# Optimization experiments

Hardware: AMD Instinct MI355X
Metric: run time of the kernel (lower is better)

Reference implementation:

```python
import jax, jax.numpy as jnp
import numpy as np

NHEAD = 8

def setup_inputs() -> dict:
    key = jax.random.key(0)
    ks = jax.random.split(key, 7)
    B, N, D = 8, 1024, 512
    scale = 1.0 / np.sqrt(D)
    return {
        "x": jax.random.normal(ks[0], (B, N, D), dtype=jnp.float32),
        "graph_bias": jax.random.normal(ks[1], (B, N, N), dtype=jnp.float32),
        "in_proj_w": jax.random.normal(ks[2], (3 * D, D), dtype=jnp.float32) * scale,
        "in_proj_b": jax.random.normal(ks[3], (3 * D,), dtype=jnp.float32) * 0.02,
        "out_proj_w": jax.random.normal(ks[4], (D, D), dtype=jnp.float32) * scale,
        "out_proj_b": jax.random.normal(ks[5], (D,), dtype=jnp.float32) * 0.02,
        "bias_strength": jnp.ones((), dtype=jnp.float32),
    }

def reference(x, graph_bias, in_proj_w, in_proj_b, out_proj_w, out_proj_b, bias_strength):
    B, N, D = x.shape
    H = NHEAD
    hd = D // H
    # fused QKV projection (matches nn.MultiheadAttention in_proj)
    qkv = x @ in_proj_w.T + in_proj_b          # (B, N, 3D)
    q, k, v = jnp.split(qkv, 3, axis=-1)
    # (B, H, N, hd)
    q = q.reshape(B, N, H, hd).transpose(0, 2, 1, 3)
    k = k.reshape(B, N, H, hd).transpose(0, 2, 1, 3)
    v = v.reshape(B, N, H, hd).transpose(0, 2, 1, 3)
    # additive bias from predicted causal structure
    alpha = jax.nn.sigmoid(bias_strength)
    causal_mask = jax.nn.sigmoid(graph_bias).transpose(0, 2, 1)   # (B, N, N)
    causal_mask = alpha * causal_mask + (1.0 - alpha) * 0.5
    attn_bias = (causal_mask - 0.5) * 10.0                        # (B, N, N)
    scores = jnp.einsum("bhqd,bhkd->bhqk", q, k) / jnp.sqrt(jnp.asarray(hd, x.dtype))
    scores = scores + attn_bias[:, None, :, :]                    # broadcast over heads
    probs = jax.nn.softmax(scores, axis=-1)
    out = jnp.einsum("bhqk,bhkd->bhqd", probs, v)                 # (B, H, N, hd)
    out = out.transpose(0, 2, 1, 3).reshape(B, N, D)
    return out @ out_proj_w.T + out_proj_b
```

## Files before the change

### kernel.cpp

```cpp
#include <hip/hip_runtime.h>

typedef __attribute__((ext_vector_type(8))) __bf16 bf16x8;
typedef __attribute__((ext_vector_type(4))) __bf16 bf16x4;
typedef __attribute__((ext_vector_type(4))) float f32x4;
typedef __attribute__((ext_vector_type(8))) _Float16 f16x8;

#define LOG2E 1.44269504088896340736f

__device__ __forceinline__ void async_load16(const void* g, void* l) {
  __builtin_amdgcn_global_load_lds(
      (const __attribute__((address_space(1))) void*)g,
      (__attribute__((address_space(3))) void*)l, 16, 0, 0);
}

__device__ __forceinline__ float fast_exp2(float x) {
#if __has_builtin(__builtin_amdgcn_exp2f)
  return __builtin_amdgcn_exp2f(x);
#else
  return __expf(x * 0.6931471805599453f);
#endif
}

__global__ void cvt3(const float* __restrict__ a, __bf16* __restrict__ oa, int na4,
                     const float* __restrict__ b, __bf16* __restrict__ ob, int nb4,
                     const float* __restrict__ c, __bf16* __restrict__ oc, int nc4) {
  int i = blockIdx.x * blockDim.x + threadIdx.x;
  int n = na4 + nb4 + nc4;
  int stride = gridDim.x * blockDim.x;
  for (; i < n; i += stride) {
    const float4* s;
    bf16x4* d;
    int j;
    if (i < na4) { s = (const float4*)a; d = (bf16x4*)oa; j = i; }
    else if (i < na4 + nb4) { s = (const float4*)b; d = (bf16x4*)ob; j = i - na4; }
    else { s = (const float4*)c; d = (bf16x4*)oc; j = i - na4 - nb4; }
    float4 v = s[j];
    bf16x4 o;
    o[0] = (__bf16)v.x; o[1] = (__bf16)v.y; o[2] = (__bf16)v.z; o[3] = (__bf16)v.w;
    d[j] = o;
  }
}

__global__ __launch_bounds__(256) void build_ebias(
    const float* __restrict__ gbias, const float* __restrict__ bstr,
    _Float16* __restrict__ ebT) {
  const int gid = blockIdx.x * 256 + threadIdx.x;
  const int lane = gid & 63;
  const int kt = (gid >> 6) & 31;
  const int qt = (gid >> 11) & 63;
  const int b = gid >> 17;
  const int g = lane >> 4, ln = lane & 15;
  const float alpha = 1.f / (1.f + __expf(-bstr[0]));
  const float bsc = 10.f * alpha * LOG2E;
  const float* base = gbias + (size_t)(b * 1024 + kt * 32 + ln) * 1024 + qt * 16 + g * 4;
  float4 va = *(const float4*)(base);
  float4 vb = *(const float4*)(base + 16 * 1024);
  float sv[8] = {va.x, va.y, va.z, va.w, vb.x, vb.y, vb.z, vb.w};
  f16x8 o;
#pragma unroll
  for (int i = 0; i < 8; ++i)
    o[i] = (_Float16)((1.f / (1.f + __expf(-sv[i])) - 0.5f) * bsc);
  *(f16x8*)(ebT + (size_t)gid * 8) = o;
}

template <int MODE>
__global__ __launch_bounds__(256) void gemm_bt(
    const __bf16* __restrict__ A, const __bf16* __restrict__ Bm,
    const float* __restrict__ bias, void* __restrict__ C0,
    __bf16* __restrict__ vT, int M, int N, int K) {
  __shared__ __align__(16) char smem[32768];
  char* lA = smem;
  char* lB = smem + 16384;
  const int t = threadIdx.x;
  const int lane = t & 63;
  const int wid = t >> 6;
  const int wm = wid >> 1, wn = wid & 1;
  const int g = lane >> 4, ln = lane & 15;
  const int m0 = blockIdx.y * 128;
  const int n0 = blockIdx.x * 128;

  const int srow = t >> 3;
  const int sswz = ((t & 7) * 16) ^ ((srow & 7) << 4);
  const size_t KB = (size_t)K * 2;
  const char* gA = (const char*)A + (size_t)m0 * KB;
  const char* gB = (const char*)Bm + (size_t)n0 * KB;

  f32x4 acc[4][4] = {};

  for (int k0 = 0; k0 < K; k0 += 64) {
    __syncthreads();
#pragma unroll
    for (int c = 0; c < 4; ++c) {
      int row = srow + 32 * c;
      async_load16(gA + (size_t)row * KB + k0 * 2 + sswz, lA + c * 4096 + t * 16);
      async_load16(gB + (size_t)row * KB + k0 * 2 + sswz, lB + c * 4096 + t * 16);
    }
    __syncthreads();
#pragma unroll
    for (int ks = 0; ks < 2; ++ks) {
      bf16x8 af[4], bf[4];
#pragma unroll
      for (int i = 0; i < 4; ++i) {
        int ar = wm * 64 + i * 16 + ln;
        int byo = (ks * 64 + g * 16) ^ ((ar & 7) << 4);
        af[i] = *(const bf16x8*)(lA + ar * 128 + byo);
        int br = wn * 64 + i * 16 + ln;
        bf[i] = *(const bf16x8*)(lB + br * 128 + byo);
      }
#pragma unroll
      for (int i = 0; i < 4; ++i)
#pragma unroll
        for (int j = 0; j < 4; ++j)
          acc[i][j] = __builtin_amdgcn_mfma_f32_16x16x32_bf16(af[i], bf[j], acc[i][j], 0, 0, 0);
    }
  }

#pragma unroll
  for (int j = 0; j < 4; ++j) {
    int col = n0 + wn * 64 + j * 16 + ln;
    float bv = bias[col];
    if (MODE == 0) {
#pragma unroll
      for (int i = 0; i < 4; ++i) {
        int row0 = m0 + wm * 64 + i * 16 + g * 4;
#pragma unroll
        for (int r = 0; r < 4; ++r)
          ((float*)C0)[(size_t)(row0 + r) * N + col] = acc[i][j][r] + bv;
      }
    } else if (col < 1024) {
      float scale = (col < 512) ? (0.125f * LOG2E) : 1.0f;
#pragma unroll
      for (int i = 0; i < 4; ++i) {
        int row0 = m0 + wm * 64 + i * 16 + g * 4;
#pragma unroll
        for (int r = 0; r < 4; ++r)
          ((__bf16*)C0)[(size_t)(row0 + r) * 1024 + col] = (__bf16)((acc[i][j][r] + bv) * scale);
      }
    } else {
      int h = (col - 1024) >> 6;
      int d = (col - 1024) & 63;
#pragma unroll
      for (int i = 0; i < 4; ++i) {
        int row0 = m0 + wm * 64 + i * 16 + g * 4;
        int b = row0 >> 10;
        bf16x4 pk;
#pragma unroll
        for (int r = 0; r < 4; ++r) pk[r] = (__bf16)(acc[i][j][r] + bv);
        *(bf16x4*)(vT + (((size_t)b * 8 + h) * 64 + d) * 1024 + (row0 & 1023)) = pk;
      }
    }
  }
}

__global__ __launch_bounds__(512, 4) void attn_fused(
    const __bf16* __restrict__ qk,
    const __bf16* __restrict__ vT,
    const _Float16* __restrict__ ebT,
    __bf16* __restrict__ attn) {
  __shared__ __align__(16) char smem[24576];
  const int t = threadIdx.x;
  const int lane = t & 63;
  const int wid = t >> 6;
  const int g = lane >> 4, ln = lane & 15;
  const int wg = ((blockIdx.x & 7) << 6) + (blockIdx.x >> 3);
  const int b = wg >> 6;
  const int rem = wg & 63;
  const int h = rem >> 3;
  const int qg = rem & 7;
  const int qt = qg * 8 + wid;
  const int q0 = qt << 4;

  char* K0 = smem;
  char* K1 = smem + 4096;
  char* V0 = smem + 8192;
  char* V1 = smem + 12288;
  char* Ps = smem + 16384 + wid * 1024;

  bf16x8 qf[2];
#pragma unroll
  for (int ks = 0; ks < 2; ++ks)
    qf[ks] = *(const bf16x8*)(qk + ((size_t)b * 1024 + q0 + ln) * 1024 +
                              h * 64 + ks * 32 + g * 8);

  float l_acc[4] = {0.f, 0.f, 0.f, 0.f};
  f32x4 o_acc[4] = {};

  const int krow = lane >> 3;
  const int ksrc = ((lane & 7) * 16) ^ (krow << 4);
  const int vrow = lane >> 2;
  const int vsrc = ((lane & 3) * 16) ^ ((vrow & 3) << 4);

  const char* qkb = (const char*)qk + (size_t)b * 1024 * 2048;
  const char* vTb = (const char*)vT + (size_t)(b * 8 + h) * 64 * 2048;
  const _Float16* ebp = ebT + (size_t)((b * 64 + qt) * 32) * 512 + lane * 8;

  auto stage = [&](int kt, char* Kd, char* Vd) {
    if (wid < 4) {
      async_load16(qkb + (size_t)(kt * 32 + wid * 8 + krow) * 2048 + 1024 + h * 128 + ksrc,
                   Kd + wid * 1024 + lane * 16);
    } else {
      int c = wid - 4;
      async_load16(vTb + (size_t)(c * 16 + vrow) * 2048 + (size_t)(kt * 32) * 2 + vsrc,
                   Vd + c * 1024 + lane * 16);
    }
  };

  stage(0, K0, V0);
  f16x8 ebc = *(const f16x8*)(ebp);
  f16x8 ebn = *(const f16x8*)(ebp + 512);
  asm volatile("s_waitcnt vmcnt(0)" ::: "memory");
  __syncthreads();

  for (int kt = 0; kt < 32; ++kt) {
    char* Kp = (kt & 1) ? K1 : K0;
    char* Vp = (kt & 1) ? V1 : V0;
    char* Kn = (kt & 1) ? K0 : K1;
    char* Vn = (kt & 1) ? V0 : V1;
    const int ktn = (kt + 1) & 31;
    const int kt2 = (kt + 2) & 31;

    stage(ktn, Kn, Vn);
    __builtin_amdgcn_sched_barrier(0);
    f16x8 ebn2 = *(const f16x8*)(ebp + (size_t)kt2 * 512);
    __builtin_amdgcn_sched_barrier(0);

    bf16x8 kf[2][2];
#pragma unroll
    for (int ni = 0; ni < 2; ++ni) {
      int br = ni * 16 + ln;
      int sw = (br & 7) << 4;
#pragma unroll
      for (int ks = 0; ks < 2; ++ks)
        kf[ni][ks] = *(const bf16x8*)(Kp + br * 128 + ((ks * 64 + g * 16) ^ sw));
    }
    bf16x8 vf[4];
#pragma unroll
    for (int di = 0; di < 4; ++di)
      vf[di] = *(const bf16x8*)(Vp + (di * 16 + ln) * 64 + ((g * 16) ^ ((ln & 3) << 4)));

    f32x4 lbf0 = {(float)ebc[0], (float)ebc[1], (float)ebc[2], (float)ebc[3]};
    f32x4 lbf1 = {(float)ebc[4], (float)ebc[5], (float)ebc[6], (float)ebc[7]};
    f32x4 s[2];
    s[0] = __builtin_amdgcn_mfma_f32_16x16x32_bf16(qf[0], kf[0][0], lbf0, 0, 0, 0);
    s[0] = __builtin_amdgcn_mfma_f32_16x16x32_bf16(qf[1], kf[0][1], s[0], 0, 0, 0);
    s[1] = __builtin_amdgcn_mfma_f32_16x16x32_bf16(qf[0], kf[1][0], lbf1, 0, 0, 0);
    s[1] = __builtin_amdgcn_mfma_f32_16x16x32_bf16(qf[1], kf[1][1], s[1], 0, 0, 0);

#pragma unroll
    for (int r = 0; r < 4; ++r) {
      float p0 = fast_exp2(s[0][r]);
      float p1 = fast_exp2(s[1][r]);
      s[0][r] = p0; s[1][r] = p1;
      l_acc[r] += p0 + p1;
    }
#pragma unroll
    for (int ni = 0; ni < 2; ++ni)
#pragma unroll
      for (int r = 0; r < 4; ++r) {
        int q = g * 4 + r;
        *(__bf16*)(Ps + q * 64 + ((ni * 32 + ln * 2) ^ (((q >> 1) & 3) << 4))) =
            (__bf16)s[ni][r];
      }
    bf16x8 pf = *(const bf16x8*)(Ps + ln * 64 + ((g * 16) ^ (((ln >> 1) & 3) << 4)));

#pragma unroll
    for (int di = 0; di < 4; ++di)
      o_acc[di] = __builtin_amdgcn_mfma_f32_16x16x32_bf16(pf, vf[di], o_acc[di], 0, 0, 0);

    asm volatile("s_waitcnt vmcnt(1)" ::: "memory");
    __builtin_amdgcn_sched_barrier(0);
    __syncthreads();
    ebc = ebn;
    ebn = ebn2;
  }

#pragma unroll
  for (int r = 0; r < 4; ++r) {
    float rs = l_acc[r];
#pragma unroll
    for (int off = 1; off < 16; off <<= 1)
      rs += __shfl_xor(rs, off, 64);
    float inv = 1.f / rs;
    int q = q0 + g * 4 + r;
#pragma unroll
    for (int di = 0; di < 4; ++di)
      attn[((size_t)b * 1024 + q) * 512 + h * 64 + di * 16 + ln] =
          (__bf16)(o_acc[di][r] * inv);
  }
}

extern "C" void kernel_launch(void* const* d_in, const int* in_sizes, int n_in,
                              void* d_out, int out_size, void* d_ws, size_t ws_size,
                              hipStream_t stream) {
  const float* x     = (const float*)d_in[0];
  const float* gb    = (const float*)d_in[1];
  const float* w_in  = (const float*)d_in[2];
  const float* b_in  = (const float*)d_in[3];
  const float* w_out = (const float*)d_in[4];
  const float* b_out = (const float*)d_in[5];
  const float* bstr  = (const float*)d_in[6];

  char* ws = (char*)d_ws;
  __bf16* qk    = (__bf16*)(ws);
  __bf16* vT    = (__bf16*)(ws + 16777216);
  __bf16* xb    = (__bf16*)(ws + 25165824);
  __bf16* w1    = (__bf16*)(ws + 33554432);
  __bf16* w2    = (__bf16*)(ws + 35127296);
  _Float16* ebT = (_Float16*)(ws + 35651584);
  __bf16* attn_buf = xb;

  cvt3<<<2560, 256, 0, stream>>>(x, xb, (8 * 1024 * 512) / 4,
                                 w_in, w1, (1536 * 512) / 4,
                                 w_out, w2, (512 * 512) / 4);
  build_ebias<<<4096, 256, 0, stream>>>(gb, bstr, ebT);

  gemm_bt<1><<<dim3(12, 64), 256, 0, stream>>>(xb, w1, b_in, qk, vT, 8192, 1536, 512);
  attn_fused<<<512, 512, 0, stream>>>(qk, vT, ebT, attn_buf);
  gemm_bt<0><<<dim3(4, 64), 256, 0, stream>>>(attn_buf, w2, b_out, d_out, nullptr, 8192, 512, 512);
}
```

Measured before the change: 96.16 us.

## Split attention key range across two wave groups and merge partial results in LDS

Each workgroup now handles 4 query tiles instead of 8, and its 8 waves split into two groups that each process half of the key tiles with their own double-buffered K/V staging. The second group writes its partial output and row sums to shared memory, and the first group adds them in before normalising and storing. The grid doubles to 1024 blocks to raise parallelism and shorten each wave's serial loop. In exchange, LDS per block grows, occupancy may drop, and K/V tiles are loaded with half the reuse across query tiles.

```diff
diff --git a/kernel.cpp b/kernel.cpp
--- a/kernel.cpp
+++ b/kernel.cpp
@@ -157,24 +157,28 @@
     const __bf16* __restrict__ vT,
     const _Float16* __restrict__ ebT,
     __bf16* __restrict__ attn) {
-  __shared__ __align__(16) char smem[24576];
+  __shared__ __align__(16) char smem[40960];
   const int t = threadIdx.x;
   const int lane = t & 63;
   const int wid = t >> 6;
   const int g = lane >> 4, ln = lane & 15;
-  const int wg = ((blockIdx.x & 7) << 6) + (blockIdx.x >> 3);
-  const int b = wg >> 6;
-  const int rem = wg & 63;
-  const int h = rem >> 3;
-  const int qg = rem & 7;
-  const int qt = qg * 8 + wid;
+  const int wg = ((blockIdx.x & 7) << 7) + (blockIdx.x >> 3);
+  const int b = wg >> 7;
+  const int rem = wg & 127;
+  const int h = rem >> 4;
+  const int qg = rem & 15;
+  const int qx = wid & 3;
+  const int kp = wid >> 2;
+  const int qt = qg * 4 + qx;
   const int q0 = qt << 4;
-
-  char* K0 = smem;
-  char* K1 = smem + 4096;
-  char* V0 = smem + 8192;
-  char* V1 = smem + 12288;
-  char* Ps = smem + 16384 + wid * 1024;
+  const int kt0 = kp * 16;
+
+  char* half = smem + kp * 16384;
+  char* K0 = half;
+  char* K1 = half + 4096;
+  char* V0 = half + 8192;
+  char* V1 = half + 12288;
+  char* Ps = smem + 32768 + wid * 1024;
 
   bf16x8 qf[2];
 #pragma unroll
@@ -194,30 +198,26 @@
   const char* vTb = (const char*)vT + (size_t)(b * 8 + h) * 64 * 2048;
   const _Float16* ebp = ebT + (size_t)((b * 64 + qt) * 32) * 512 + lane * 8;
 
-  auto stage = [&](int kt, char* Kd, char* Vd) {
-    if (wid < 4) {
-      async_load16(qkb + (size_t)(kt * 32 + wid * 8 + krow) * 2048 + 1024 + h * 128 + ksrc,
-                   Kd + wid * 1024 + lane * 16);
-    } else {
-      int c = wid - 4;
-      async_load16(vTb + (size_t)(c * 16 + vrow) * 2048 + (size_t)(kt * 32) * 2 + vsrc,
-                   Vd + c * 1024 + lane * 16);
-    }
+  auto stage = [&](int ktg, char* Kd, char* Vd) {
+    async_load16(qkb + (size_t)(ktg * 32 + qx * 8 + krow) * 2048 + 1024 + h * 128 + ksrc,
+                 Kd + qx * 1024 + lane * 16);
+    async_load16(vTb + (size_t)(qx * 16 + vrow) * 2048 + (size_t)(ktg * 32) * 2 + vsrc,
+                 Vd + qx * 1024 + lane * 16);
   };
 
-  stage(0, K0, V0);
-  f16x8 ebc = *(const f16x8*)(ebp);
-  f16x8 ebn = *(const f16x8*)(ebp + 512);
+  stage(kt0, K0, V0);
+  f16x8 ebc = *(const f16x8*)(ebp + (size_t)kt0 * 512);
+  f16x8 ebn = *(const f16x8*)(ebp + (size_t)(kt0 + 1) * 512);
   asm volatile("s_waitcnt vmcnt(0)" ::: "memory");
   __syncthreads();
 
-  for (int kt = 0; kt < 32; ++kt) {
+  for (int kt = 0; kt < 16; ++kt) {
     char* Kp = (kt & 1) ? K1 : K0;
     char* Vp = (kt & 1) ? V1 : V0;
     char* Kn = (kt & 1) ? K0 : K1;
     char* Vn = (kt & 1) ? V0 : V1;
-    const int ktn = (kt + 1) & 31;
-    const int kt2 = (kt + 2) & 31;
+    const int ktn = kt0 + ((kt + 1) & 15);
+    const int kt2 = kt0 + ((kt + 2) & 15);
 
     stage(ktn, Kn, Vn);
     __builtin_amdgcn_sched_barrier(0);
@@ -274,18 +274,40 @@
     ebn = ebn2;
   }
 
-#pragma unroll
-  for (int r = 0; r < 4; ++r) {
-    float rs = l_acc[r];
-#pragma unroll
-    for (int off = 1; off < 16; off <<= 1)
-      rs += __shfl_xor(rs, off, 64);
-    float inv = 1.f / rs;
-    int q = q0 + g * 4 + r;
+  if (kp == 1) {
+    char* dst = smem + 16384 + qx * 4096;
 #pragma unroll
     for (int di = 0; di < 4; ++di)
-      attn[((size_t)b * 1024 + q) * 512 + h * 64 + di * 16 + ln] =
-          (__bf16)(o_acc[di][r] * inv);
+      *(f32x4*)(dst + di * 1024 + lane * 16) = o_acc[di];
+    f32x4 lv = {l_acc[0], l_acc[1], l_acc[2], l_acc[3]};
+    *(f32x4*)(Ps + lane * 16) = lv;
+  }
+  __syncthreads();
+  if (kp == 0) {
+    const char* src = smem + 16384 + qx * 4096;
+#pragma unroll
+    for (int di = 0; di < 4; ++di) {
+      f32x4 ov = *(const f32x4*)(src + di * 1024 + lane * 16);
+#pragma unroll
+      for (int r = 0; r < 4; ++r) o_acc[di][r] += ov[r];
+    }
+    f32x4 lv = *(const f32x4*)(smem + 32768 + (wid + 4) * 1024 + lane * 16);
+#pragma unroll
+    for (int r = 0; r < 4; ++r) l_acc[r] += lv[r];
+
+#pragma unroll
+    for (int r = 0; r < 4; ++r) {
+      float rs = l_acc[r];
+#pragma unroll
+      for (int off = 1; off < 16; off <<= 1)
+        rs += __shfl_xor(rs, off, 64);
+      float inv = 1.f / rs;
+      int q = q0 + g * 4 + r;
+#pragma unroll
+      for (int di = 0; di < 4; ++di)
+        attn[((size_t)b * 1024 + q) * 512 + h * 64 + di * 16 + ln] =
+            (__bf16)(o_acc[di][r] * inv);
+    }
   }
 }
 
@@ -315,6 +337,6 @@
   build_ebias<<<4096, 256, 0, stream>>>(gb, bstr, ebT);
 
   gemm_bt<1><<<dim3(12, 64), 256, 0, stream>>>(xb, w1, b_in, qk, vT, 8192, 1536, 512);
-  attn_fused<<<512, 512, 0, stream>>>(qk, vT, ebT, attn_buf);
+  attn_fused<<<1024, 512, 0, stream>>>(qk, vT, ebT, attn_buf);
   gemm_bt<0><<<dim3(4, 64), 256, 0, stream>>>(attn_buf, w2, b_out, d_out, nullptr, 8192, 512, 512);
 }
```

Result: slower. 99.68 us (+3.7%).
